# Performance work log

Hardware: AMD Instinct MI355X
Metric: run time of the kernel (lower is better)

The kernel has to match this reference:

```python
import jax, jax.numpy as jnp
import numpy as np

B, T, C, H = 2, 2048, 1024, 16
D = C // H  # d_head = 64


def setup_inputs() -> dict:
    key = jax.random.key(0)
    k1, k2, k3 = jax.random.split(key, 3)
    x = jax.random.normal(k1, (B, T, C), dtype=jnp.float32)
    # torch Linear weights stored pre-transposed as [in, out] so we apply x @ W
    w_qkv = jax.random.normal(k2, (C, 3 * C), dtype=jnp.float32) * (C ** -0.5)
    w_out = jax.random.normal(k3, (C, C), dtype=jnp.float32) * (C ** -0.5)
    charge_w = jnp.array([0.0, 3.0, 6.0], dtype=jnp.float32)  # CHARGES init
    # causal mask, broadcast over batch and heads; mask==0 positions are blocked
    mask = jnp.tril(jnp.ones((1, 1, T, T), dtype=jnp.int32))
    return {"x": x, "mask": mask, "w_qkv": w_qkv, "w_out": w_out, "charge_w": charge_w}


def reference(x, mask, w_qkv, w_out, charge_w):
    B, T, C = x.shape
    H = 16
    D = C // H
    qkv = (x @ w_qkv).reshape(B, T, 3, H, D)
    q, k, v = qkv[:, :, 0], qkv[:, :, 1], qkv[:, :, 2]  # each [B,T,H,D]
    scale = D ** -0.5
    attn = jnp.einsum("bqhd,bkhd->bhqk", q, k) * scale  # [B,H,T,T]
    charge_bias = jnp.mod(jnp.sum(charge_w), 9.0) * 0.001  # scalar bias
    attn = attn + charge_bias
    attn = jnp.where(mask == 0, jnp.float32(-1e9), attn)
    attn = jax.nn.softmax(attn, axis=-1)  # dropout is identity in eval mode
    out = jnp.einsum("bhqk,bkhd->bqhd", attn, v).reshape(B, T, C)
    return out @ w_out
```

## Files before the change

### kernel.cpp

```cpp
#include <hip/hip_runtime.h>
#include <stdint.h>


typedef __attribute__((ext_vector_type(4))) float f32x4;
typedef __attribute__((ext_vector_type(16))) float f32x16;
typedef __attribute__((ext_vector_type(8))) __bf16 bf16x8;
typedef __attribute__((ext_vector_type(8))) unsigned short ushort8;
typedef __attribute__((ext_vector_type(4))) unsigned short ushort4v;
typedef __attribute__((ext_vector_type(4))) unsigned int uint4v;

#define DEV __device__ __forceinline__

DEV unsigned short f32_to_bf16(float f) {
    union { float f; unsigned int u; } cv; cv.f = f;
    unsigned int u = cv.u;
    return (unsigned short)((u + 0x7FFFu + ((u >> 16) & 1u)) >> 16);
}

DEV bf16x8 load_bf16x8(const unsigned short* p) {
    ushort8 v = *(const ushort8*)p;
    return __builtin_bit_cast(bf16x8, v);
}

DEV unsigned cvt_pk_bf16(float lo, float hi) {
    unsigned r;
    asm("v_cvt_pk_bf16_f32 %0, %1, %2" : "=v"(r) : "v"(lo), "v"(hi));
    return r;
}

DEV void gload_lds16(const void* g, void* l) {
    __builtin_amdgcn_global_load_lds(
        (const __attribute__((address_space(1))) unsigned int*)g,
        (__attribute__((address_space(3))) unsigned int*)l, 16, 0, 0);
}

DEV f32x16 vzero16() {
    f32x16 v;
#pragma unroll
    for (int i = 0; i < 16; ++i) v[i] = 0.f;
    return v;
}

__global__ void cvt_kernel(const float* __restrict__ in, unsigned short* __restrict__ out, int n) {
    int i = (blockIdx.x * blockDim.x + threadIdx.x) * 4;
    if (i >= n) return;
    f32x4 v = *(const f32x4*)(in + i);
    ushort4v o;
    o[0] = f32_to_bf16(v[0]); o[1] = f32_to_bf16(v[1]);
    o[2] = f32_to_bf16(v[2]); o[3] = f32_to_bf16(v[3]);
    *(ushort4v*)(out + i) = o;
}

__global__ __launch_bounds__(256) void tcvt_kernel(const float* __restrict__ in,
                                                   unsigned short* __restrict__ out,
                                                   int R, int Cn) {
    __shared__ float tl[32][33];
    const int tx = threadIdx.x & 31, ty = threadIdx.x >> 5;
    const int c0 = blockIdx.x * 32, r0 = blockIdx.y * 32;
#pragma unroll
    for (int rr = 0; rr < 4; ++rr) {
        int r = ty + rr * 8;
        tl[r][tx] = in[(size_t)(r0 + r) * Cn + c0 + tx];
    }
    __syncthreads();
#pragma unroll
    for (int rr = 0; rr < 4; ++rr) {
        int cc = ty + rr * 8;
        out[(size_t)(c0 + cc) * R + r0 + tx] = f32_to_bf16(tl[tx][cc]);
    }
}

template<bool OUT_BF16, bool SCALE_Q>
__global__ __launch_bounds__(256) void gemm_kernel(
    const unsigned short* __restrict__ A,
    const unsigned short* __restrict__ Bt,
    void* __restrict__ C, int K, int ldc)
{
    __shared__ __align__(16) unsigned short As[128 * 32];
    __shared__ __align__(16) unsigned short Bs[128 * 32];

    const int tid = threadIdx.x;
    const int lane = tid & 63;
    const int w = tid >> 6;
    const int wr = w >> 1, wc = w & 1;
    const int g = lane >> 4, ci = lane & 15;
    const int bx = blockIdx.x, by = blockIdx.y;

    f32x4 acc[4][4];
#pragma unroll
    for (int i = 0; i < 4; ++i)
#pragma unroll
        for (int j = 0; j < 4; ++j) acc[i][j] = f32x4{0.f, 0.f, 0.f, 0.f};

    for (int k0 = 0; k0 < K; k0 += 32) {
        __syncthreads();
#pragma unroll
        for (int i = 0; i < 2; ++i) {
            int off = i * 4096 + w * 1024 + lane * 16;
            int row = off >> 6;
            int cch = (off >> 4) & 3;
            gload_lds16(A  + (size_t)(by * 128 + row) * K + k0 + cch * 8,
                        (char*)As + i * 4096 + w * 1024);
            gload_lds16(Bt + (size_t)(bx * 128 + row) * K + k0 + cch * 8,
                        (char*)Bs + i * 4096 + w * 1024);
        }
        __syncthreads();

        bf16x8 af[4], bfr[4];
#pragma unroll
        for (int mf = 0; mf < 4; ++mf) af[mf]  = load_bf16x8(&As[(wr * 64 + mf * 16 + ci) * 32 + g * 8]);
#pragma unroll
        for (int nf = 0; nf < 4; ++nf) bfr[nf] = load_bf16x8(&Bs[(wc * 64 + nf * 16 + ci) * 32 + g * 8]);
#pragma unroll
        for (int mf = 0; mf < 4; ++mf)
#pragma unroll
            for (int nf = 0; nf < 4; ++nf)
                acc[mf][nf] = __builtin_amdgcn_mfma_f32_16x16x32_bf16(af[mf], bfr[nf], acc[mf][nf], 0, 0, 0);
    }

#pragma unroll
    for (int mf = 0; mf < 4; ++mf)
#pragma unroll
        for (int nf = 0; nf < 4; ++nf)
#pragma unroll
            for (int r = 0; r < 4; ++r) {
                int row = by * 128 + wr * 64 + mf * 16 + g * 4 + r;
                int col = bx * 128 + wc * 64 + nf * 16 + ci;
                float v = acc[mf][nf][r];
                if (SCALE_Q && col < 1024) v *= 0.1803368801f;
                if (OUT_BF16)
                    ((unsigned short*)C)[(size_t)row * ldc + col] = f32_to_bf16(v);
                else
                    ((float*)C)[(size_t)row * ldc + col] = v;
            }
}

__global__ __launch_bounds__(256) void attn3_kernel(const unsigned short* __restrict__ qkv,
                                                    unsigned short* __restrict__ attn) {
    constexpr int T = 2048, HD3 = 3072, Cc = 1024;
    __shared__ __align__(16) unsigned short Ks[3][4096];
    __shared__ __align__(16) unsigned short Vt[2][4096];

    const int tid = threadIdx.x;
    const int lane = tid & 63;
    const int w = tid >> 6;
    const int l31 = lane & 31;
    const int hi = lane >> 5;

    const int bx = blockIdx.x;
    const int qb = 15 - (bx >> 5);
    const int bh = bx & 31;
    const int h = bh & 15;
    const int b = bh >> 4;
    const int q0w = qb * 128 + w * 32;
    const int qrow = q0w + l31;
    const size_t base = (size_t)b * T * HD3;

    bf16x8 qf[4];
#pragma unroll
    for (int t = 0; t < 4; ++t)
        qf[t] = load_bf16x8(qkv + base + (size_t)qrow * HD3 + h * 64 + t * 16 + hi * 8);

    f32x16 acc0 = vzero16(), acc1 = vzero16();
    float m = -3e38f, l = 0.f;
    const int nt = 2 * qb + 2;

    ushort8 vA0, vA1, vB0, vB1;
#define LOADV(tile, r0, r1) do { int kv0_ = (tile) * 64; \
    int rr0_ = tid >> 3, cc0_ = tid & 7; \
    r0 = *(const ushort8*)(qkv + base + (size_t)(kv0_ + rr0_) * HD3 + 2 * Cc + h * 64 + cc0_ * 8); \
    int c1_ = 256 + tid; int rr1_ = c1_ >> 3, cc1_ = c1_ & 7; \
    r1 = *(const ushort8*)(qkv + base + (size_t)(kv0_ + rr1_) * HD3 + 2 * Cc + h * 64 + cc1_ * 8); } while (0)

#define DMAK(tile, kb) do { int kv0_ = (tile) * 64; \
    _Pragma("unroll") for (int i_ = 0; i_ < 2; ++i_) { \
        int off_ = i_ * 4096 + w * 1024 + lane * 16; \
        int row_ = off_ >> 7; \
        int csw_ = ((lane & 7) * 8) ^ ((row_ & 7) * 8); \
        gload_lds16(qkv + base + (size_t)(kv0_ + row_) * HD3 + Cc + h * 64 + csw_, \
                    (void*)(((char*)&Ks[kb][0]) + i_ * 4096 + w * 1024)); } } while (0)

#define WRITEV(vb, r0, r1) do { \
    _Pragma("unroll") for (int i_ = 0; i_ < 2; ++i_) { \
        int c_ = i_ * 256 + tid; int row_ = c_ >> 3, cc_ = c_ & 7; \
        ushort8 v_ = i_ ? r1 : r0; \
        _Pragma("unroll") for (int j_ = 0; j_ < 8; ++j_) { \
            int d_ = cc_ * 8 + j_; \
            int sw_ = ((d_ ^ (d_ >> 3)) & 7) * 8; \
            Vt[vb][d_ * 64 + (row_ ^ sw_)] = v_[j_]; } } } while (0)

    LOADV(0, vA0, vA1);
    DMAK(0, 0);
    asm volatile("s_waitcnt vmcnt(0)" ::: "memory");
    __builtin_amdgcn_sched_barrier(0);
    WRITEV(0, vA0, vA1);
    LOADV(1, vB0, vB1);
    DMAK(1, 1);
    asm volatile("s_waitcnt lgkmcnt(0)" ::: "memory");
    __builtin_amdgcn_sched_barrier(0);
    __builtin_amdgcn_s_barrier();
    __builtin_amdgcn_sched_barrier(0);

    for (int t = 0; t < nt; ++t) {
        const int kv0 = t * 64;
        const int kcur = t % 3;
        const int vcur = t & 1;
        const bool act = (kv0 <= q0w + 31);
        const bool pre2 = (t + 2) < nt;

        if (pre2) {
            if (t & 1) LOADV(t + 2, vB0, vB1); else LOADV(t + 2, vA0, vA1);
            DMAK(t + 2, (t + 2) % 3);
        }

        f32x16 s0 = vzero16(), s1 = vzero16();
        bf16x8 pf[4];
        if (act) {
            const bool st1_ok = (kv0 + 32 <= q0w + 31);
            __builtin_amdgcn_s_setprio(1);
#pragma unroll
            for (int tt = 0; tt < 4; ++tt) {
                int row = l31;
                int idx = kcur * 4096 + row * 64 + ((tt * 16 + hi * 8) ^ ((row & 7) * 8));
                s0 = __builtin_amdgcn_mfma_f32_32x32x16_bf16(load_bf16x8(&Ks[0][idx]), qf[tt], s0, 0, 0, 0);
            }
            if (st1_ok) {
#pragma unroll
                for (int tt = 0; tt < 4; ++tt) {
                    int row = 32 + l31;
                    int idx = kcur * 4096 + row * 64 + ((tt * 16 + hi * 8) ^ ((row & 7) * 8));
                    s1 = __builtin_amdgcn_mfma_f32_32x32x16_bf16(load_bf16x8(&Ks[0][idx]), qf[tt], s1, 0, 0, 0);
                }
            }
            __builtin_amdgcn_s_setprio(0);
            const bool needmask = (kv0 + 63 > q0w);
            if (needmask) {
#pragma unroll
                for (int G = 0; G < 4; ++G)
#pragma unroll
                    for (int rr = 0; rr < 4; ++rr) {
                        int kvb = kv0 + 8 * G + 4 * hi + rr;
                        s0[G * 4 + rr] = (kvb      <= qrow) ? s0[G * 4 + rr] : -3e38f;
                        s1[G * 4 + rr] = (kvb + 32 <= qrow) ? s1[G * 4 + rr] : -3e38f;
                    }
            }
            float pmax = -3e38f;
#pragma unroll
            for (int i = 0; i < 16; ++i) pmax = fmaxf(pmax, fmaxf(s0[i], s1[i]));
            pmax = fmaxf(pmax, __shfl_xor(pmax, 32));
            if (!__all(pmax - m <= 11.5f)) {
                float mnew = fmaxf(m, pmax);
                float alpha = exp2f(m - mnew);
                m = mnew;
                l *= alpha;
#pragma unroll
                for (int i = 0; i < 16; ++i) { acc0[i] *= alpha; acc1[i] *= alpha; }
            }
            float rs = 0.f;
#pragma unroll
            for (int i = 0; i < 16; ++i) {
                s0[i] = exp2f(s0[i] - m);
                s1[i] = exp2f(s1[i] - m);
                rs += s0[i] + s1[i];
            }
            rs += __shfl_xor(rs, 32);
            l += rs;

            unsigned pk0[4][2], pk1[4][2];
#pragma unroll
            for (int G = 0; G < 4; ++G) {
                pk0[G][0] = cvt_pk_bf16(s0[G * 4 + 0], s0[G * 4 + 1]);
                pk0[G][1] = cvt_pk_bf16(s0[G * 4 + 2], s0[G * 4 + 3]);
                pk1[G][0] = cvt_pk_bf16(s1[G * 4 + 0], s1[G * 4 + 1]);
                pk1[G][1] = cvt_pk_bf16(s1[G * 4 + 2], s1[G * 4 + 3]);
            }
#pragma unroll
            for (int tf = 0; tf < 4; ++tf) {
                const int kb = tf & 1;
                unsigned sA0, sA1, sB0, sB1;
                if (tf < 2) { sA0 = pk0[2 * kb][0]; sA1 = pk0[2 * kb][1]; sB0 = pk0[2 * kb + 1][0]; sB1 = pk0[2 * kb + 1][1]; }
                else        { sA0 = pk1[2 * kb][0]; sA1 = pk1[2 * kb][1]; sB0 = pk1[2 * kb + 1][0]; sB1 = pk1[2 * kb + 1][1]; }
                unsigned sd0 = hi ? sA0 : sB0, sd1 = hi ? sA1 : sB1;
                unsigned rc0 = (unsigned)__shfl_xor((int)sd0, 32);
                unsigned rc1 = (unsigned)__shfl_xor((int)sd1, 32);
                uint4v u;
                u[0] = hi ? rc0 : sA0;  u[1] = hi ? rc1 : sA1;
                u[2] = hi ? sB0 : rc0;  u[3] = hi ? sB1 : rc1;
                pf[tf] = __builtin_bit_cast(bf16x8, u);
            }
        }

        if (t + 1 < nt) {
            if (t & 1) WRITEV(vcur ^ 1, vA0, vA1); else WRITEV(vcur ^ 1, vB0, vB1);
        }

        if (act) {
            __builtin_amdgcn_s_setprio(1);
#pragma unroll
            for (int tt = 0; tt < 4; ++tt) {
                {
                    int d = l31, sw = ((d ^ (d >> 3)) & 7) * 8;
                    bf16x8 vf = load_bf16x8(&Vt[vcur][d * 64 + ((tt * 16 + hi * 8) ^ sw)]);
                    acc0 = __builtin_amdgcn_mfma_f32_32x32x16_bf16(vf, pf[tt], acc0, 0, 0, 0);
                }
                {
                    int d = 32 + l31, sw = ((d ^ (d >> 3)) & 7) * 8;
                    bf16x8 vf = load_bf16x8(&Vt[vcur][d * 64 + ((tt * 16 + hi * 8) ^ sw)]);
                    acc1 = __builtin_amdgcn_mfma_f32_32x32x16_bf16(vf, pf[tt], acc1, 0, 0, 0);
                }
            }
            __builtin_amdgcn_s_setprio(0);
        }

        if (pre2) asm volatile("s_waitcnt vmcnt(4) lgkmcnt(0)" ::: "memory");
        else      asm volatile("s_waitcnt vmcnt(0) lgkmcnt(0)" ::: "memory");
        __builtin_amdgcn_sched_barrier(0);
        __builtin_amdgcn_s_barrier();
        __builtin_amdgcn_sched_barrier(0);
    }

    const float invl = 1.0f / l;
    const size_t ob = (size_t)b * T * Cc + (size_t)qrow * Cc + h * 64;
#pragma unroll
    for (int G = 0; G < 4; ++G) {
        ushort4v o0, o1;
#pragma unroll
        for (int rr = 0; rr < 4; ++rr) {
            o0[rr] = f32_to_bf16(acc0[G * 4 + rr] * invl);
            o1[rr] = f32_to_bf16(acc1[G * 4 + rr] * invl);
        }
        int d0 = 8 * G + 4 * hi;
        *(ushort4v*)(attn + ob + d0) = o0;
        *(ushort4v*)(attn + ob + 32 + d0) = o1;
    }
#undef LOADV
#undef DMAK
#undef WRITEV
}

extern "C" void kernel_launch(void* const* d_in, const int* in_sizes, int n_in,
                              void* d_out, int out_size, void* d_ws, size_t ws_size,
                              hipStream_t stream) {
    const float* x     = (const float*)d_in[0];
    const float* w_qkv = (const float*)d_in[2];
    const float* w_out = (const float*)d_in[3];
    float* out = (float*)d_out;

    unsigned short* xb     = (unsigned short*)d_ws;
    unsigned short* wqkvT  = xb + 4194304;
    unsigned short* woutT  = wqkvT + 3145728;
    unsigned short* qkv    = woutT + 1048576;
    unsigned short* attn   = qkv + 12582912;

    cvt_kernel<<<4096, 256, 0, stream>>>(x, xb, 4194304);
    tcvt_kernel<<<dim3(96, 32), 256, 0, stream>>>(w_qkv, wqkvT, 1024, 3072);
    tcvt_kernel<<<dim3(32, 32), 256, 0, stream>>>(w_out, woutT, 1024, 1024);

    gemm_kernel<true, true><<<dim3(24, 32), 256, 0, stream>>>(xb, wqkvT, (void*)qkv, 1024, 3072);

    attn3_kernel<<<512, 256, 0, stream>>>(qkv, attn);

    gemm_kernel<false, false><<<dim3(8, 32), 256, 0, stream>>>(attn, woutT, (void*)out, 1024, 1024);
}
```

Before: 162.6 us.

## Double-buffer GEMM LDS loads and restructure attention block order and softmax reductions

```diff
diff --git a/kernel.cpp b/kernel.cpp
--- a/kernel.cpp
+++ b/kernel.cpp
@@ -39,6 +39,27 @@
 #pragma unroll
     for (int i = 0; i < 16; ++i) v[i] = 0.f;
     return v;
+}
+
+DEV float tmax32(const f32x16& a, const f32x16& b) {
+    float m[16];
+#pragma unroll
+    for (int i = 0; i < 16; ++i) m[i] = fmaxf(a[i], b[i]);
+#pragma unroll
+    for (int st = 8; st > 0; st >>= 1)
+#pragma unroll
+        for (int i = 0; i < 8; ++i) if (i < st) m[i] = fmaxf(m[i], m[i + st]);
+    return m[0];
+}
+DEV float tsum32(const f32x16& a, const f32x16& b) {
+    float m[16];
+#pragma unroll
+    for (int i = 0; i < 16; ++i) m[i] = a[i] + b[i];
+#pragma unroll
+    for (int st = 8; st > 0; st >>= 1)
+#pragma unroll
+        for (int i = 0; i < 8; ++i) if (i < st) m[i] = m[i] + m[i + st];
+    return m[0];
 }
 
 __global__ void cvt_kernel(const float* __restrict__ in, unsigned short* __restrict__ out, int n) {
@@ -76,8 +97,8 @@
     const unsigned short* __restrict__ Bt,
     void* __restrict__ C, int K, int ldc)
 {
-    __shared__ __align__(16) unsigned short As[128 * 32];
-    __shared__ __align__(16) unsigned short Bs[128 * 32];
+    __shared__ __align__(16) unsigned short As[2][4096];
+    __shared__ __align__(16) unsigned short Bs[2][4096];
 
     const int tid = threadIdx.x;
     const int lane = tid & 63;
@@ -85,6 +106,17 @@
     const int wr = w >> 1, wc = w & 1;
     const int g = lane >> 4, ci = lane & 15;
     const int bx = blockIdx.x, by = blockIdx.y;
+    const int soff = w * 1024 + lane * 16;
+    const int srow = soff >> 6;
+    const int scch = (soff >> 4) & 3;
+
+#define GSTAGE(buf, k0_) do { \
+    _Pragma("unroll") for (int i_ = 0; i_ < 2; ++i_) { \
+        int row_ = srow + i_ * 64; \
+        gload_lds16(A  + (size_t)(by * 128 + row_) * K + (k0_) + scch * 8, \
+                    (char*)As[buf] + i_ * 4096 + w * 1024); \
+        gload_lds16(Bt + (size_t)(bx * 128 + row_) * K + (k0_) + scch * 8, \
+                    (char*)Bs[buf] + i_ * 4096 + w * 1024); } } while (0)
 
     f32x4 acc[4][4];
 #pragma unroll
@@ -92,31 +124,34 @@
 #pragma unroll
         for (int j = 0; j < 4; ++j) acc[i][j] = f32x4{0.f, 0.f, 0.f, 0.f};
 
-    for (int k0 = 0; k0 < K; k0 += 32) {
-        __syncthreads();
-#pragma unroll
-        for (int i = 0; i < 2; ++i) {
-            int off = i * 4096 + w * 1024 + lane * 16;
-            int row = off >> 6;
-            int cch = (off >> 4) & 3;
-            gload_lds16(A  + (size_t)(by * 128 + row) * K + k0 + cch * 8,
-                        (char*)As + i * 4096 + w * 1024);
-            gload_lds16(Bt + (size_t)(bx * 128 + row) * K + k0 + cch * 8,
-                        (char*)Bs + i * 4096 + w * 1024);
-        }
-        __syncthreads();
+    GSTAGE(0, 0);
+    asm volatile("s_waitcnt vmcnt(0)" ::: "memory");
+    __builtin_amdgcn_sched_barrier(0);
+    __builtin_amdgcn_s_barrier();
+    __builtin_amdgcn_sched_barrier(0);
+
+    const int nk = K >> 5;
+    for (int kt = 0; kt < nk; ++kt) {
+        const int cur = kt & 1;
+        if (kt + 1 < nk) GSTAGE(cur ^ 1, (kt + 1) << 5);
 
         bf16x8 af[4], bfr[4];
 #pragma unroll
-        for (int mf = 0; mf < 4; ++mf) af[mf]  = load_bf16x8(&As[(wr * 64 + mf * 16 + ci) * 32 + g * 8]);
-#pragma unroll
-        for (int nf = 0; nf < 4; ++nf) bfr[nf] = load_bf16x8(&Bs[(wc * 64 + nf * 16 + ci) * 32 + g * 8]);
+        for (int mf = 0; mf < 4; ++mf) af[mf]  = load_bf16x8(&As[cur][(wr * 64 + mf * 16 + ci) * 32 + g * 8]);
+#pragma unroll
+        for (int nf = 0; nf < 4; ++nf) bfr[nf] = load_bf16x8(&Bs[cur][(wc * 64 + nf * 16 + ci) * 32 + g * 8]);
 #pragma unroll
         for (int mf = 0; mf < 4; ++mf)
 #pragma unroll
             for (int nf = 0; nf < 4; ++nf)
                 acc[mf][nf] = __builtin_amdgcn_mfma_f32_16x16x32_bf16(af[mf], bfr[nf], acc[mf][nf], 0, 0, 0);
-    }
+
+        asm volatile("s_waitcnt vmcnt(0) lgkmcnt(0)" ::: "memory");
+        __builtin_amdgcn_sched_barrier(0);
+        __builtin_amdgcn_s_barrier();
+        __builtin_amdgcn_sched_barrier(0);
+    }
+#undef GSTAGE
 
 #pragma unroll
     for (int mf = 0; mf < 4; ++mf)
@@ -135,7 +170,7 @@
             }
 }
 
-__global__ __launch_bounds__(256) void attn3_kernel(const unsigned short* __restrict__ qkv,
+__global__ __launch_bounds__(256) void attn4_kernel(const unsigned short* __restrict__ qkv,
                                                     unsigned short* __restrict__ attn) {
     constexpr int T = 2048, HD3 = 3072, Cc = 1024;
     __shared__ __align__(16) unsigned short Ks[3][4096];
@@ -148,7 +183,7 @@
     const int hi = lane >> 5;
 
     const int bx = blockIdx.x;
-    const int qb = 15 - (bx >> 5);
+    const int qb = (bx < 256) ? (15 - (bx >> 5)) : ((bx - 256) >> 5);
     const int bh = bx & 31;
     const int h = bh & 15;
     const int b = bh >> 4;
@@ -208,14 +243,17 @@
         const bool act = (kv0 <= q0w + 31);
         const bool pre2 = (t + 2) < nt;
 
+        if (t + 1 < nt) {
+            if (t & 1) WRITEV(vcur ^ 1, vA0, vA1); else WRITEV(vcur ^ 1, vB0, vB1);
+        }
         if (pre2) {
             if (t & 1) LOADV(t + 2, vB0, vB1); else LOADV(t + 2, vA0, vA1);
             DMAK(t + 2, (t + 2) % 3);
         }
 
-        f32x16 s0 = vzero16(), s1 = vzero16();
-        bf16x8 pf[4];
         if (act) {
+            f32x16 s0 = vzero16(), s1 = vzero16();
+            bf16x8 pf[4];
             const bool st1_ok = (kv0 + 32 <= q0w + 31);
             __builtin_amdgcn_s_setprio(1);
 #pragma unroll
@@ -244,9 +282,7 @@
                         s1[G * 4 + rr] = (kvb + 32 <= qrow) ? s1[G * 4 + rr] : -3e38f;
                     }
             }
-            float pmax = -3e38f;
-#pragma unroll
-            for (int i = 0; i < 16; ++i) pmax = fmaxf(pmax, fmaxf(s0[i], s1[i]));
+            float pmax = tmax32(s0, s1);
             pmax = fmaxf(pmax, __shfl_xor(pmax, 32));
             if (!__all(pmax - m <= 11.5f)) {
                 float mnew = fmaxf(m, pmax);
@@ -256,15 +292,11 @@
 #pragma unroll
                 for (int i = 0; i < 16; ++i) { acc0[i] *= alpha; acc1[i] *= alpha; }
             }
-            float rs = 0.f;
 #pragma unroll
             for (int i = 0; i < 16; ++i) {
                 s0[i] = exp2f(s0[i] - m);
                 s1[i] = exp2f(s1[i] - m);
-                rs += s0[i] + s1[i];
-            }
-            rs += __shfl_xor(rs, 32);
-            l += rs;
+            }
 
             unsigned pk0[4][2], pk1[4][2];
 #pragma unroll
@@ -288,13 +320,7 @@
                 u[2] = hi ? sB0 : rc0;  u[3] = hi ? sB1 : rc1;
                 pf[tf] = __builtin_bit_cast(bf16x8, u);
             }
-        }
-
-        if (t + 1 < nt) {
-            if (t & 1) WRITEV(vcur ^ 1, vA0, vA1); else WRITEV(vcur ^ 1, vB0, vB1);
-        }
-
-        if (act) {
+
             __builtin_amdgcn_s_setprio(1);
 #pragma unroll
             for (int tt = 0; tt < 4; ++tt) {
@@ -310,6 +336,9 @@
                 }
             }
             __builtin_amdgcn_s_setprio(0);
+
+            float rsum = tsum32(s0, s1);
+            l += rsum + __shfl_xor(rsum, 32);
         }
 
         if (pre2) asm volatile("s_waitcnt vmcnt(4) lgkmcnt(0)" ::: "memory");
@@ -358,7 +387,7 @@
 
     gemm_kernel<true, true><<<dim3(24, 32), 256, 0, stream>>>(xb, wqkvT, (void*)qkv, 1024, 3072);
 
-    attn3_kernel<<<512, 256, 0, stream>>>(qkv, attn);
+    attn4_kernel<<<512, 256, 0, stream>>>(qkv, attn);
 
     gemm_kernel<false, false><<<dim3(8, 32), 256, 0, stream>>>(attn, woutT, (void*)out, 1024, 1024);
 }
```

Measured after the change: 156.0 us. -4.0%, faster.
